# Kernel tuning notes

Hardware: AMD Instinct MI355X
Metric: run time of the kernel (lower is better)

Reference implementation:

```python
import jax, jax.numpy as jnp
import numpy as np

SLOPE = 25.0   # snntorch surrogate.fast_sigmoid default slope
THR = 1.0      # snntorch Leaky default threshold
BETA = 0.95
SPIKE_STEPS = 4
NUM_HEADS = 16

@jax.custom_vjp
def spike(u):
    # Heaviside forward, fast-sigmoid surrogate backward
    return (u > 0).astype(u.dtype)

def _spike_fwd(u):
    return spike(u), u

def _spike_bwd(u, g):
    return (g / (SLOPE * jnp.abs(u) + 1.0) ** 2,)

spike.defvjp(_spike_fwd, _spike_bwd)

def lif_mean(cur):
    """Run SPIKE_STEPS of a snntorch Leaky neuron (subtract reset, detached)
    with constant input current `cur`; return mean spike train over time."""
    def step(mem, _):
        reset = jax.lax.stop_gradient(spike(mem - THR))
        mem = BETA * mem + cur - reset * THR
        return mem, spike(mem - THR)
    _, spk = jax.lax.scan(step, jnp.zeros_like(cur), None, length=SPIKE_STEPS)
    return spk.mean(axis=0)

def setup_inputs() -> dict:
    B, S, D = 2, 2048, 1024
    key = jax.random.key(0)
    ks = jax.random.split(key, 9)
    std = 1.0 / np.sqrt(D)
    mkw = lambda k: jax.random.uniform(k, (D, D), jnp.float32, -std, std)
    mkb = lambda k: jax.random.uniform(k, (D,), jnp.float32, -std, std)
    return {
        "x": jax.random.normal(ks[0], (B, S, D), jnp.float32),
        "q_w": mkw(ks[1]), "q_b": mkb(ks[2]),
        "k_w": mkw(ks[3]), "k_b": mkb(ks[4]),
        "v_w": mkw(ks[5]), "v_b": mkb(ks[6]),
        "o_w": mkw(ks[7]), "o_b": mkb(ks[8]),
    }

def reference(x, q_w, q_b, k_w, k_b, v_w, v_b, o_w, o_b):
    B, S, D = x.shape
    H = NUM_HEADS
    Hd = D // H
    # projections -> [B, H, S, Hd]  (weights stored [in, out])
    proj = lambda w, b: (x @ w + b).reshape(B, S, H, Hd).transpose(0, 2, 1, 3)
    q, k, v = proj(q_w, q_b), proj(k_w, k_b), proj(v_w, v_b)
    # LIF spiking recurrence, aggregated over time
    q_agg, k_agg, v_agg = lif_mean(q), lif_mean(k), lif_mean(v)
    # standard scaled dot-product attention on aggregated spikes
    scores = jnp.einsum('bhqd,bhkd->bhqk', q_agg, k_agg) / jnp.sqrt(jnp.float32(Hd))
    attn = jax.nn.softmax(scores, axis=-1)
    out = jnp.einsum('bhqk,bhkd->bhqd', attn, v_agg)
    out = out.transpose(0, 2, 1, 3).reshape(B, S, D)
    return out @ o_w + o_b
```

## Files before the change

kernel.cpp:

```cpp
#include <hip/hip_runtime.h>
#include <hip/hip_bf16.h>
#include <stdint.h>

typedef unsigned short u16;
typedef unsigned int u32;
typedef __bf16 bf16x8 __attribute__((ext_vector_type(8)));
typedef float f32x4 __attribute__((ext_vector_type(4)));

#define B_   2
#define S_   2048
#define D_   1024
#define H_   16
#define HD_  64

__device__ __forceinline__ u16 f2bf(float f) {
    u32 u = __float_as_uint(f);
    u32 r = (u + 0x7FFFu + ((u >> 16) & 1u)) >> 16;
    return (u16)r;
}
__device__ __forceinline__ float bf2f(u16 s) { return __uint_as_float(((u32)s) << 16); }

__device__ __forceinline__ f32x4 mfma16(bf16x8 a, bf16x8 b, f32x4 c) {
    return __builtin_amdgcn_mfma_f32_16x16x32_bf16(a, b, c, 0, 0, 0);
}

__device__ __forceinline__ void gl16(const u16* g, u16* l) {
    __builtin_amdgcn_global_load_lds(
        (const __attribute__((address_space(1))) void*)g,
        (__attribute__((address_space(3))) void*)l, 16, 0, 0);
}

__global__ void convert_x_kernel(const float* __restrict__ x,
                                 u16* __restrict__ o, int n4) {
    int i = blockIdx.x * blockDim.x + threadIdx.x;
    if (i >= n4) return;
    float4 v = reinterpret_cast<const float4*>(x)[i];
    uint2 hp;
    hp.x = (u32)f2bf(v.x) | ((u32)f2bf(v.y) << 16);
    hp.y = (u32)f2bf(v.z) | ((u32)f2bf(v.w) << 16);
    reinterpret_cast<uint2*>(o)[i] = hp;
}

__global__ void trans_w_kernel(const float* __restrict__ qw, const float* __restrict__ kw,
                               const float* __restrict__ vw, const float* __restrict__ ow,
                               u16* __restrict__ thi_all) {
    __shared__ float tile[32][33];
    const int z = blockIdx.z;
    const float* w = (z == 0) ? qw : (z == 1) ? kw : (z == 2) ? vw : ow;
    u16* thi = thi_all + (size_t)z * 1048576;
    int bi = blockIdx.y;
    int bj = blockIdx.x;
    int tx = threadIdx.x;
    int ty = threadIdx.y;
#pragma unroll
    for (int k = 0; k < 4; k++) {
        int r = ty + k * 8;
        tile[r][tx] = w[(size_t)(bi * 32 + r) * D_ + bj * 32 + tx];
    }
    __syncthreads();
#pragma unroll
    for (int k = 0; k < 4; k++) {
        int r = ty + k * 8;
        thi[(size_t)(bj * 32 + r) * D_ + bi * 32 + tx] = f2bf(tile[tx][r]);
    }
}

__global__ __launch_bounds__(256, 3)
void qkv_gemm(const u16* __restrict__ Ag, const u16* __restrict__ Bg,
              const float* __restrict__ qb, const float* __restrict__ kb,
              const float* __restrict__ vb,
              u16* __restrict__ o0, u16* __restrict__ o1, u16* __restrict__ o2) {
    __shared__ __align__(16) u16 lA[2][128 * 32];
    __shared__ __align__(16) u16 lB[2][128 * 32];

    const int t = threadIdx.x;
    const int flat = blockIdx.y * 24 + blockIdx.x;
    const int swz = (flat & 7) * 96 + (flat >> 3);
    const int m0 = (swz / 24) * 128;
    const int n0 = (swz % 24) * 128;
    const int wid = t >> 6, lane = t & 63;
    const int wm = wid >> 1, wn = wid & 1;
    const int lr = lane & 15, lg = lane >> 4;

    f32x4 acc[4][4] = {};

    auto STAGE = [&](int buf, int kk) {
        const int k0 = kk * 32;
#pragma unroll
        for (int p = 0; p < 2; p++) {
            int idx = p * 256 + wid * 64 + lane;
            int row = idx >> 2, sl = idx & 3;
            int slx = sl ^ ((row >> 1) & 3);
            gl16(Ag + (size_t)(m0 + row) * D_ + k0 + slx * 8,
                 &lA[buf][(p * 256 + wid * 64) * 8]);
            gl16(Bg + (size_t)(n0 + row) * D_ + k0 + slx * 8,
                 &lB[buf][(p * 256 + wid * 64) * 8]);
        }
    };

    STAGE(0, 0);
    __syncthreads();
    int cur = 0;

    for (int kk = 0; kk < 32; ++kk) {
        if (kk < 31) STAGE(cur ^ 1, kk + 1);

        bf16x8 af[4], bf[4];
#pragma unroll
        for (int m = 0; m < 4; m++) {
            int row = wm * 64 + m * 16 + lr;
            af[m] = *reinterpret_cast<const bf16x8*>(
                &lA[cur][row * 32 + (lg ^ ((row >> 1) & 3)) * 8]);
        }
#pragma unroll
        for (int n = 0; n < 4; n++) {
            int row = wn * 64 + n * 16 + lr;
            bf[n] = *reinterpret_cast<const bf16x8*>(
                &lB[cur][row * 32 + (lg ^ ((row >> 1) & 3)) * 8]);
        }
#pragma unroll
        for (int m = 0; m < 4; m++)
#pragma unroll
            for (int n = 0; n < 4; n++)
                acc[m][n] = mfma16(af[m], bf[n], acc[m][n]);

        __syncthreads();
        cur ^= 1;
    }

    const int col0f = n0 + wn * 64;
    const int proj = col0f >> 10;
    const float* bp = (proj == 0) ? qb : (proj == 1) ? kb : vb;
    u16* dst = (proj == 0) ? o0 : (proj == 1) ? o1 : o2;
#pragma unroll
    for (int m = 0; m < 4; m++) {
#pragma unroll
        for (int n = 0; n < 4; n++) {
#pragma unroll
            for (int r = 0; r < 4; r++) {
                int row = m0 + wm * 64 + m * 16 + lg * 4 + r;
                int colp = (col0f + n * 16 + lr) & 1023;
                float cur_i = acc[m][n][r] + bp[colp];
                float mem = 0.f;
                int cnt = 0;
#pragma unroll
                for (int tt = 0; tt < 4; tt++) {
                    float reset = (mem > 1.f) ? 1.f : 0.f;
                    mem = 0.95f * mem;
                    mem = mem + cur_i;
                    mem = mem - reset;
                    cnt += (mem > 1.f) ? 1 : 0;
                }
                u16 agg = (u16)(__float_as_uint((float)cnt * 0.25f) >> 16);
                int b = row >> 11, s = row & 2047;
                int h = colp >> 6, d = colp & 63;
                size_t idx;
                if (proj == 2)
                    idx = ((size_t)(b * H_ + h) * HD_ + d) * S_ + s;
                else
                    idx = ((size_t)(b * H_ + h) * S_ + s) * HD_ + d;
                dst[idx] = agg;
            }
        }
    }
}

__global__ __launch_bounds__(256, 4)
void o_gemm(const u16* __restrict__ Ag, const u16* __restrict__ Bhg,
            const float* __restrict__ bias, float* __restrict__ out) {
    __shared__ __align__(16) u16 lA[2][64 * 32];
    __shared__ __align__(16) u16 lB[2][64 * 32];

    const int t = threadIdx.x;
    const int flat = blockIdx.y * 16 + blockIdx.x;
    const int swz = (flat & 7) * 128 + (flat >> 3);
    const int m0 = (swz >> 4) * 64;
    const int n0 = (swz & 15) * 64;
    const int wid = t >> 6, lane = t & 63;
    const int wm = wid >> 1, wn = wid & 1;
    const int lr = lane & 15, lg = lane >> 4;

    f32x4 acc[2][2] = {};

    auto STAGE = [&](int buf, int kk) {
        const int k0 = kk * 32;
        int idx = wid * 64 + lane;
        int row = idx >> 2, sl = idx & 3;
        int slx = sl ^ ((row >> 1) & 3);
        gl16(Ag + (size_t)(m0 + row) * D_ + k0 + slx * 8,
             &lA[buf][(wid * 64) * 8]);
        gl16(Bhg + (size_t)(n0 + row) * D_ + k0 + slx * 8,
             &lB[buf][(wid * 64) * 8]);
    };

    STAGE(0, 0);
    __syncthreads();
    int cur = 0;

    for (int kk = 0; kk < 32; ++kk) {
        if (kk < 31) STAGE(cur ^ 1, kk + 1);

        bf16x8 af[2], bf[2];
#pragma unroll
        for (int m = 0; m < 2; m++) {
            int row = wm * 32 + m * 16 + lr;
            af[m] = *reinterpret_cast<const bf16x8*>(
                &lA[cur][row * 32 + (lg ^ ((row >> 1) & 3)) * 8]);
        }
#pragma unroll
        for (int n = 0; n < 2; n++) {
            int row = wn * 32 + n * 16 + lr;
            bf[n] = *reinterpret_cast<const bf16x8*>(
                &lB[cur][row * 32 + (lg ^ ((row >> 1) & 3)) * 8]);
        }
#pragma unroll
        for (int m = 0; m < 2; m++)
#pragma unroll
            for (int n = 0; n < 2; n++)
                acc[m][n] = mfma16(af[m], bf[n], acc[m][n]);

        __syncthreads();
        cur ^= 1;
    }

#pragma unroll
    for (int m = 0; m < 2; m++)
#pragma unroll
        for (int n = 0; n < 2; n++)
#pragma unroll
            for (int r = 0; r < 4; r++) {
                int row = m0 + wm * 32 + m * 16 + lg * 4 + r;
                int col = n0 + wn * 32 + n * 16 + lr;
                out[(size_t)row * D_ + col] = acc[m][n][r] + bias[col];
            }
}

__global__ __launch_bounds__(256, 3)
void attn_kernel(const u16* __restrict__ qa, const u16* __restrict__ ka,
                 const u16* __restrict__ vt, u16* __restrict__ oag) {
    __shared__ __align__(16) u16 Kb[2][64 * 64];
    __shared__ __align__(16) u16 Vb[2][64 * 64];
    __shared__ __align__(16) u16 Pt[4][32 * 64];

    const int t = threadIdx.x;
    const int wid = t >> 6, lane = t & 63;
    const int lr = lane & 15, lg = lane >> 4;

    const int flat = blockIdx.y * 16 + blockIdx.x;
    const int swz = (flat & 7) * 64 + (flat >> 3);
    const int bh = swz >> 4;
    const int q0 = (swz & 15) * 128;

    const u16* qbase = qa + (size_t)bh * S_ * HD_;
    const u16* kbase = ka + (size_t)bh * S_ * HD_;
    const u16* vbase = vt + (size_t)bh * HD_ * S_;

    bf16x8 qf[2][2];
#pragma unroll
    for (int m = 0; m < 2; m++)
#pragma unroll
        for (int kc = 0; kc < 2; kc++) {
            int row = q0 + wid * 32 + m * 16 + lr;
            qf[m][kc] = *reinterpret_cast<const bf16x8*>(
                qbase + (size_t)row * HD_ + kc * 32 + lg * 8);
        }

    bf16x8 ones;
#pragma unroll
    for (int j = 0; j < 8; j++) ones[j] = (__bf16)1.0f;

    f32x4 oacc[2][4] = {};
    f32x4 ssum[2] = {};
    u16* myP = &Pt[wid][0];

    auto STAGE = [&](int buf, int kt) {
#pragma unroll
        for (int p = 0; p < 2; p++) {
            int slot = p * 256 + wid * 64 + lane;
            int row = slot >> 3, sl = slot & 7;
            int slx = sl ^ (row & 7);
            gl16(kbase + (size_t)(kt * 64 + row) * HD_ + slx * 8,
                 &Kb[buf][(p * 256 + wid * 64) * 8]);
            gl16(vbase + (size_t)row * S_ + kt * 64 + slx * 8,
                 &Vb[buf][(p * 256 + wid * 64) * 8]);
        }
    };

    STAGE(0, 0);
    __syncthreads();
    int cur = 0;

    for (int kt = 0; kt < 32; ++kt) {
        if (kt < 31) STAGE(cur ^ 1, kt + 1);

        f32x4 sacc[2][4] = {};
        __builtin_amdgcn_s_setprio(1);
#pragma unroll
        for (int n = 0; n < 4; n++) {
            int row = n * 16 + lr;
#pragma unroll
            for (int kc = 0; kc < 2; kc++) {
                int sl = kc * 4 + lg;
                bf16x8 kb = *reinterpret_cast<const bf16x8*>(
                    &Kb[cur][row * 64 + ((sl ^ (row & 7)) * 8)]);
                sacc[0][n] = mfma16(qf[0][kc], kb, sacc[0][n]);
                sacc[1][n] = mfma16(qf[1][kc], kb, sacc[1][n]);
            }
        }
        __builtin_amdgcn_s_setprio(0);
        char* pbase = reinterpret_cast<char*>(myP);
#pragma unroll
        for (int m = 0; m < 2; m++)
#pragma unroll
            for (int n = 0; n < 4; n++) {
                float pv[4];
#pragma unroll
                for (int r = 0; r < 4; r++) {
                    float tt = __builtin_fmaf(sacc[m][n][r], 0.18033688f,
                                              -5.7707802f);
                    asm("v_exp_f32 %0, %1" : "=v"(pv[r]) : "v"(tt));
                }
                u32 d01, d23;
                asm("v_cvt_pk_bf16_f32 %0, %1, %2"
                    : "=v"(d01) : "v"(pv[0]), "v"(pv[1]));
                asm("v_cvt_pk_bf16_f32 %0, %1, %2"
                    : "=v"(d23) : "v"(pv[2]), "v"(pv[3]));
                const int pr = m * 16 + lg * 4;
                const int cb = (n * 16 + lr) * 2;
                *reinterpret_cast<u16*>(pbase + (pr + 0) * 128 +
                                        (cb ^ (((pr + 0) & 7) << 4))) = (u16)d01;
                *reinterpret_cast<u16*>(pbase + (pr + 1) * 128 +
                                        (cb ^ (((pr + 1) & 7) << 4))) = (u16)(d01 >> 16);
                *reinterpret_cast<u16*>(pbase + (pr + 2) * 128 +
                                        (cb ^ (((pr + 2) & 7) << 4))) = (u16)d23;
                *reinterpret_cast<u16*>(pbase + (pr + 3) * 128 +
                                        (cb ^ (((pr + 3) & 7) << 4))) = (u16)(d23 >> 16);
            }
        bf16x8 pa[2][2];
#pragma unroll
        for (int m = 0; m < 2; m++)
#pragma unroll
            for (int kc = 0; kc < 2; kc++) {
                int row = m * 16 + lr;
                int sl = kc * 4 + lg;
                pa[m][kc] = *reinterpret_cast<const bf16x8*>(
                    &myP[row * 64 + ((sl ^ (row & 7)) * 8)]);
            }
        __builtin_amdgcn_s_setprio(1);
#pragma unroll
        for (int n = 0; n < 4; n++) {
            int row = n * 16 + lr;
#pragma unroll
            for (int kc = 0; kc < 2; kc++) {
                int sl = kc * 4 + lg;
                bf16x8 vb = *reinterpret_cast<const bf16x8*>(
                    &Vb[cur][row * 64 + ((sl ^ (row & 7)) * 8)]);
                oacc[0][n] = mfma16(pa[0][kc], vb, oacc[0][n]);
                oacc[1][n] = mfma16(pa[1][kc], vb, oacc[1][n]);
            }
        }
        ssum[0] = mfma16(pa[0][0], ones, ssum[0]);
        ssum[0] = mfma16(pa[0][1], ones, ssum[0]);
        ssum[1] = mfma16(pa[1][0], ones, ssum[1]);
        ssum[1] = mfma16(pa[1][1], ones, ssum[1]);
        __builtin_amdgcn_s_setprio(0);

        __syncthreads();
        cur ^= 1;
    }

    const int b = bh >> 4, h = bh & 15;
#pragma unroll
    for (int m = 0; m < 2; m++)
#pragma unroll
        for (int n = 0; n < 4; n++)
#pragma unroll
            for (int r = 0; r < 4; r++) {
                int q = q0 + wid * 32 + m * 16 + lg * 4 + r;
                int d = n * 16 + lr;
                float v = oacc[m][n][r] / ssum[m][r];
                oag[(size_t)(b * S_ + q) * D_ + h * 64 + d] = f2bf(v);
            }
}

extern "C" void kernel_launch(void* const* d_in, const int* in_sizes, int n_in,
                              void* d_out, int out_size, void* d_ws, size_t ws_size,
                              hipStream_t stream) {
    (void)in_sizes; (void)n_in; (void)out_size; (void)ws_size;
    const float* x  = (const float*)d_in[0];
    const float* qw = (const float*)d_in[1];
    const float* qb = (const float*)d_in[2];
    const float* kw = (const float*)d_in[3];
    const float* kb = (const float*)d_in[4];
    const float* vw = (const float*)d_in[5];
    const float* vb = (const float*)d_in[6];
    const float* ow = (const float*)d_in[7];
    const float* ob = (const float*)d_in[8];

    u16* ws = (u16*)d_ws;
    const size_t C = 4194304;
    u16* xbf = ws + 0 * C;
    u16* wt  = ws + 1 * C;
    u16* qag = ws + 2 * C;
    u16* kag = ws + 3 * C;
    u16* vtg = ws + 4 * C;
    u16* oag = ws + 5 * C;

    convert_x_kernel<<<4096, 256, 0, stream>>>(x, xbf, (int)(C / 4));
    trans_w_kernel<<<dim3(32, 32, 4), dim3(32, 8), 0, stream>>>(
        qw, kw, vw, ow, wt);

    qkv_gemm<<<dim3(24, 32), 256, 0, stream>>>(
        xbf, wt, qb, kb, vb, qag, kag, vtg);
    attn_kernel<<<dim3(16, 32), 256, 0, stream>>>(qag, kag, vtg, oag);
    o_gemm<<<dim3(16, 64), 256, 0, stream>>>(
        oag, wt + 3 * 1048576, ob, (float*)d_out);
}
```

Before: 127.7 us.

## Re-tile attention warps as 2x2 q/key grid and merge prep kernels

After: 130.8 us. 1.02x slower.

```diff
diff --git a/kernel.cpp b/kernel.cpp
--- a/kernel.cpp
+++ b/kernel.cpp
@@ -30,28 +30,29 @@
         (__attribute__((address_space(3))) void*)l, 16, 0, 0);
 }
 
-__global__ void convert_x_kernel(const float* __restrict__ x,
-                                 u16* __restrict__ o, int n4) {
-    int i = blockIdx.x * blockDim.x + threadIdx.x;
-    if (i >= n4) return;
-    float4 v = reinterpret_cast<const float4*>(x)[i];
-    uint2 hp;
-    hp.x = (u32)f2bf(v.x) | ((u32)f2bf(v.y) << 16);
-    hp.y = (u32)f2bf(v.z) | ((u32)f2bf(v.w) << 16);
-    reinterpret_cast<uint2*>(o)[i] = hp;
-}
-
-__global__ void trans_w_kernel(const float* __restrict__ qw, const float* __restrict__ kw,
-                               const float* __restrict__ vw, const float* __restrict__ ow,
-                               u16* __restrict__ thi_all) {
+__global__ void prep_kernel(const float* __restrict__ x,
+                            const float* __restrict__ qw, const float* __restrict__ kw,
+                            const float* __restrict__ vw, const float* __restrict__ ow,
+                            u16* __restrict__ xbf, u16* __restrict__ wt_all) {
     __shared__ float tile[32][33];
-    const int z = blockIdx.z;
+    const int bid = blockIdx.x;
+    const int t = threadIdx.x;
+    if (bid < 4096) {
+        int i = bid * 256 + t;
+        float4 v = reinterpret_cast<const float4*>(x)[i];
+        uint2 hp;
+        hp.x = (u32)f2bf(v.x) | ((u32)f2bf(v.y) << 16);
+        hp.y = (u32)f2bf(v.z) | ((u32)f2bf(v.w) << 16);
+        reinterpret_cast<uint2*>(xbf)[i] = hp;
+        return;
+    }
+    const int f = bid - 4096;
+    const int z = f >> 10;
+    const int bi = (f & 1023) >> 5;
+    const int bj = f & 31;
     const float* w = (z == 0) ? qw : (z == 1) ? kw : (z == 2) ? vw : ow;
-    u16* thi = thi_all + (size_t)z * 1048576;
-    int bi = blockIdx.y;
-    int bj = blockIdx.x;
-    int tx = threadIdx.x;
-    int ty = threadIdx.y;
+    u16* thi = wt_all + (size_t)z * 1048576;
+    const int tx = t & 31, ty = t >> 5;
 #pragma unroll
     for (int k = 0; k < 4; k++) {
         int r = ty + k * 8;
@@ -240,10 +241,12 @@
                  const u16* __restrict__ vt, u16* __restrict__ oag) {
     __shared__ __align__(16) u16 Kb[2][64 * 64];
     __shared__ __align__(16) u16 Vb[2][64 * 64];
-    __shared__ __align__(16) u16 Pt[4][32 * 64];
+    __shared__ __align__(16) u16 Pt[2][64 * 64];
 
     const int t = threadIdx.x;
     const int wid = t >> 6, lane = t & 63;
+    const int wq = wid >> 1;
+    const int wk = wid & 1;
     const int lr = lane & 15, lg = lane >> 4;
 
     const int flat = blockIdx.y * 16 + blockIdx.x;
@@ -255,12 +258,12 @@
     const u16* kbase = ka + (size_t)bh * S_ * HD_;
     const u16* vbase = vt + (size_t)bh * HD_ * S_;
 
-    bf16x8 qf[2][2];
-#pragma unroll
-    for (int m = 0; m < 2; m++)
+    bf16x8 qf[4][2];
+#pragma unroll
+    for (int m = 0; m < 4; m++)
 #pragma unroll
         for (int kc = 0; kc < 2; kc++) {
-            int row = q0 + wid * 32 + m * 16 + lr;
+            int row = q0 + wq * 64 + m * 16 + lr;
             qf[m][kc] = *reinterpret_cast<const bf16x8*>(
                 qbase + (size_t)row * HD_ + kc * 32 + lg * 8);
         }
@@ -269,9 +272,9 @@
 #pragma unroll
     for (int j = 0; j < 8; j++) ones[j] = (__bf16)1.0f;
 
-    f32x4 oacc[2][4] = {};
-    f32x4 ssum[2] = {};
-    u16* myP = &Pt[wid][0];
+    f32x4 oacc[4][2] = {};
+    f32x4 ssum[4] = {};
+    u16* myP = &Pt[wq][0];
 
     auto STAGE = [&](int buf, int kt) {
 #pragma unroll
@@ -293,26 +296,27 @@
     for (int kt = 0; kt < 32; ++kt) {
         if (kt < 31) STAGE(cur ^ 1, kt + 1);
 
-        f32x4 sacc[2][4] = {};
+        f32x4 sacc[4][2] = {};
         __builtin_amdgcn_s_setprio(1);
 #pragma unroll
-        for (int n = 0; n < 4; n++) {
-            int row = n * 16 + lr;
+        for (int n = 0; n < 2; n++) {
+            int row = wk * 32 + n * 16 + lr;
 #pragma unroll
             for (int kc = 0; kc < 2; kc++) {
                 int sl = kc * 4 + lg;
                 bf16x8 kb = *reinterpret_cast<const bf16x8*>(
                     &Kb[cur][row * 64 + ((sl ^ (row & 7)) * 8)]);
-                sacc[0][n] = mfma16(qf[0][kc], kb, sacc[0][n]);
-                sacc[1][n] = mfma16(qf[1][kc], kb, sacc[1][n]);
+#pragma unroll
+                for (int m = 0; m < 4; m++)
+                    sacc[m][n] = mfma16(qf[m][kc], kb, sacc[m][n]);
             }
         }
         __builtin_amdgcn_s_setprio(0);
         char* pbase = reinterpret_cast<char*>(myP);
 #pragma unroll
-        for (int m = 0; m < 2; m++)
-#pragma unroll
-            for (int n = 0; n < 4; n++) {
+        for (int m = 0; m < 4; m++)
+#pragma unroll
+            for (int n = 0; n < 2; n++) {
                 float pv[4];
 #pragma unroll
                 for (int r = 0; r < 4; r++) {
@@ -326,7 +330,7 @@
                 asm("v_cvt_pk_bf16_f32 %0, %1, %2"
                     : "=v"(d23) : "v"(pv[2]), "v"(pv[3]));
                 const int pr = m * 16 + lg * 4;
-                const int cb = (n * 16 + lr) * 2;
+                const int cb = (wk * 32 + n * 16 + lr) * 2;
                 *reinterpret_cast<u16*>(pbase + (pr + 0) * 128 +
                                         (cb ^ (((pr + 0) & 7) << 4))) = (u16)d01;
                 *reinterpret_cast<u16*>(pbase + (pr + 1) * 128 +
@@ -336,9 +340,11 @@
                 *reinterpret_cast<u16*>(pbase + (pr + 3) * 128 +
                                         (cb ^ (((pr + 3) & 7) << 4))) = (u16)(d23 >> 16);
             }
-        bf16x8 pa[2][2];
-#pragma unroll
-        for (int m = 0; m < 2; m++)
+        asm volatile("s_waitcnt lgkmcnt(0)\n\ts_barrier" ::: "memory");
+
+        bf16x8 pa[4][2];
+#pragma unroll
+        for (int m = 0; m < 4; m++)
 #pragma unroll
             for (int kc = 0; kc < 2; kc++) {
                 int row = m * 16 + lr;
@@ -348,21 +354,23 @@
             }
         __builtin_amdgcn_s_setprio(1);
 #pragma unroll
-        for (int n = 0; n < 4; n++) {
-            int row = n * 16 + lr;
+        for (int n = 0; n < 2; n++) {
+            int row = wk * 32 + n * 16 + lr;
 #pragma unroll
             for (int kc = 0; kc < 2; kc++) {
                 int sl = kc * 4 + lg;
                 bf16x8 vb = *reinterpret_cast<const bf16x8*>(
                     &Vb[cur][row * 64 + ((sl ^ (row & 7)) * 8)]);
-                oacc[0][n] = mfma16(pa[0][kc], vb, oacc[0][n]);
-                oacc[1][n] = mfma16(pa[1][kc], vb, oacc[1][n]);
-            }
-        }
-        ssum[0] = mfma16(pa[0][0], ones, ssum[0]);
-        ssum[0] = mfma16(pa[0][1], ones, ssum[0]);
-        ssum[1] = mfma16(pa[1][0], ones, ssum[1]);
-        ssum[1] = mfma16(pa[1][1], ones, ssum[1]);
+#pragma unroll
+                for (int m = 0; m < 4; m++)
+                    oacc[m][n] = mfma16(pa[m][kc], vb, oacc[m][n]);
+            }
+        }
+#pragma unroll
+        for (int m = 0; m < 4; m++) {
+            ssum[m] = mfma16(pa[m][0], ones, ssum[m]);
+            ssum[m] = mfma16(pa[m][1], ones, ssum[m]);
+        }
         __builtin_amdgcn_s_setprio(0);
 
         __syncthreads();
@@ -371,13 +379,13 @@
 
     const int b = bh >> 4, h = bh & 15;
 #pragma unroll
-    for (int m = 0; m < 2; m++)
-#pragma unroll
-        for (int n = 0; n < 4; n++)
+    for (int m = 0; m < 4; m++)
+#pragma unroll
+        for (int n = 0; n < 2; n++)
 #pragma unroll
             for (int r = 0; r < 4; r++) {
-                int q = q0 + wid * 32 + m * 16 + lg * 4 + r;
-                int d = n * 16 + lr;
+                int q = q0 + wq * 64 + m * 16 + lg * 4 + r;
+                int d = wk * 32 + n * 16 + lr;
                 float v = oacc[m][n][r] / ssum[m][r];
                 oag[(size_t)(b * S_ + q) * D_ + h * 64 + d] = f2bf(v);
             }
@@ -406,9 +414,7 @@
     u16* vtg = ws + 4 * C;
     u16* oag = ws + 5 * C;
 
-    convert_x_kernel<<<4096, 256, 0, stream>>>(x, xbf, (int)(C / 4));
-    trans_w_kernel<<<dim3(32, 32, 4), dim3(32, 8), 0, stream>>>(
-        qw, kw, vw, ow, wt);
+    prep_kernel<<<8192, 256, 0, stream>>>(x, qw, kw, vw, ow, xbf, wt);
 
     qkv_gemm<<<dim3(24, 32), 256, 0, stream>>>(
         xbf, wt, qb, kb, vb, qag, kag, vtg);
```
